# Optimization experiments

Measured on AMD Instinct MI355X. Metric: run time of the kernel, lower is better.

The kernel has to match this reference:

```python
import jax, jax.numpy as jnp
import numpy as np

LPB = 0.03   # lower_probability_bound
LEB = 0.2    # lower_entropy_bound
UEB = 0.5    # upper_entropy_bound
BETA = 1.0
N, K, S, D = 8192, 1000, 8, 1024


def setup_inputs() -> dict:
    key = jax.random.key(0)
    k1, k2, k3 = jax.random.split(key, 3)
    x = jax.random.normal(k1, (N, D), dtype=jnp.float32)
    # per-sample logit temperature so entropies spread across the gating band
    base = jax.random.normal(k2, (N, K), dtype=jnp.float32)
    scales = jax.random.uniform(k3, (N, 1), dtype=jnp.float32, minval=1.0, maxval=15.0)
    text_logits = base * scales
    memory = jnp.zeros((K, S, D), dtype=jnp.float32)
    # init_entropy(prop_max=1): -log(1/K) = log(K)
    memory_entropy = jnp.full((K, S), jnp.log(jnp.float32(K)), dtype=jnp.float32)
    memory_state = jnp.zeros((K, S), dtype=bool)
    return {"x": x, "text_logits": text_logits, "memory": memory,
            "memory_entropy": memory_entropy, "memory_state": memory_state}


def _update_memory(memory, memory_entropy, memory_state, x, text_logits):
    """Sequential entropy-gated scatter update (order-dependent, as in torch loop)."""
    def step(carry, inp):
        mem, ent, st = carry
        xi, li = inp                      # xi: [D], li: [K]
        p = jax.nn.softmax(li)
        lab = jnp.argmax(li)
        H = -jnp.sum(jnp.log(p + 1e-6) * p)  # shannon entropy
        row = ent[lab]                    # [S] entropies of this class's slots
        cond = (p[lab] > LPB) & (H > LEB) & (H < UEB) & jnp.any(H < row)
        idx = jnp.argmax(row)             # evict highest-entropy slot
        mem = mem.at[lab, idx].set(jnp.where(cond, xi, mem[lab, idx]))
        ent = ent.at[lab, idx].set(jnp.where(cond, H, ent[lab, idx]))
        st = st.at[lab, idx].set(jnp.where(cond, True, st[lab, idx]))
        return (mem, ent, st), cond

    (mem, ent, st), selected = jax.lax.scan(
        step, (memory, memory_entropy, memory_state), (x, text_logits))
    return mem, ent, st, selected


def reference(x, text_logits, memory, memory_entropy, memory_state):
    mem, ent, st, selected = _update_memory(memory, memory_entropy, memory_state, x, text_logits)
    # get_logits: A_ = (memory @ x.T).permute(2,0,1) -> [N, K, S]
    A_ = jnp.einsum('ksd,nd->nks', mem, x)
    logits = -jnp.sum(jnp.exp(-BETA * (1.0 - A_)), axis=-1)  # [N, K]
    return logits
```

## Files before the change

### kernel.cpp

```cpp
#include <hip/hip_runtime.h>
#include <hip/hip_bf16.h>
#include <math.h>

#define NN 8192
#define KK 1000
#define SS 8
#define DD 1024
#define RR (KK * SS)
#define RRP 8192

typedef __bf16 bf16x8 __attribute__((ext_vector_type(8)));
typedef float f32x4 __attribute__((ext_vector_type(4)));
typedef unsigned short ushort_t;
typedef ushort_t ushort8 __attribute__((ext_vector_type(8)));

static __device__ __forceinline__ ushort_t f2bf(float f) {
  unsigned u = __float_as_uint(f);
  unsigned r = (u + 0x7FFFu + ((u >> 16) & 1u)) >> 16;
  return (ushort_t)r;
}

#define GLD16(gsrc, ldst)                                                     \
  __builtin_amdgcn_global_load_lds(                                           \
      (const __attribute__((address_space(1))) unsigned int*)(gsrc),          \
      (__attribute__((address_space(3))) unsigned int*)(ldst), 16, 0, 0)

#define SBAR() asm volatile("s_barrier" ::: "memory")
#define WAITVM(n) asm volatile("s_waitcnt vmcnt(" #n ")" ::: "memory")

__global__ __launch_bounds__(256) void stats_kernel(
    const float* __restrict__ tl, int2* __restrict__ cand) {
  __shared__ float sv[KK];
  __shared__ float redv[256];
  __shared__ int   redi[256];
  const int n = blockIdx.x;
  const int t = threadIdx.x;
  const float* row = tl + (size_t)n * KK;
  for (int j = t; j < KK; j += 256) sv[j] = row[j];
  __syncthreads();

  float bv = -INFINITY; int bi = KK;
  for (int j = t; j < KK; j += 256) { float v = sv[j]; if (v > bv) { bv = v; bi = j; } }
  redv[t] = bv; redi[t] = bi;
  __syncthreads();
  for (int off = 128; off > 0; off >>= 1) {
    if (t < off) {
      float ov = redv[t + off]; int oi = redi[t + off];
      if (ov > redv[t] || (ov == redv[t] && oi < redi[t])) { redv[t] = ov; redi[t] = oi; }
    }
    __syncthreads();
  }
  const float m = redv[0];
  const int lab = redi[0];
  __syncthreads();

  float z = 0.f;
  for (int j = t; j < KK; j += 256) z += expf(sv[j] - m);
  redv[t] = z;
  __syncthreads();
  for (int off = 128; off > 0; off >>= 1) {
    if (t < off) redv[t] += redv[t + off];
    __syncthreads();
  }
  const float Z = redv[0];
  __syncthreads();

  float h = 0.f;
  for (int j = t; j < KK; j += 256) {
    float p = expf(sv[j] - m) / Z;
    h -= p * logf(p + 1e-6f);
  }
  redv[t] = h;
  __syncthreads();
  for (int off = 128; off > 0; off >>= 1) {
    if (t < off) redv[t] += redv[t + off];
    __syncthreads();
  }
  if (t == 0) {
    const float H = redv[0];
    const float plab = 1.0f / Z;
    const bool c = (plab > 0.03f) && (H > 0.2f) && (H < 0.5f);
    cand[n] = make_int2(c ? lab : -1, __float_as_int(H));
  }
}

__global__ __launch_bounds__(256) void select_kernel(
    const int2* __restrict__ cand, const float* __restrict__ ment,
    int* __restrict__ sel) {
  const int w = threadIdx.x >> 6;
  const int l = threadIdx.x & 63;
  const int k = blockIdx.x * 4 + w;
  if (k >= KK) return;

  float ent[SS]; int idx[SS];
  #pragma unroll
  for (int s = 0; s < SS; ++s) { ent[s] = ment[k * SS + s]; idx[s] = -1; }

  for (int base = 0; base < NN; base += 64) {
    const int2 c = cand[base + l];
    unsigned long long msk = __ballot(c.x == k);
    while (msk) {
      const int src = __ffsll((long long)msk) - 1;
      msk &= msk - 1;
      const float H = __shfl(__int_as_float(c.y), src);
      float mx = ent[0]; int mi = 0;
      #pragma unroll
      for (int s = 1; s < SS; ++s) if (ent[s] > mx) { mx = ent[s]; mi = s; }
      if (H < mx) { ent[mi] = H; idx[mi] = base + src; }
    }
  }
  if (l == 0) {
    #pragma unroll
    for (int s = 0; s < SS; ++s) sel[k * SS + s] = idx[s];
  }
}

__global__ __launch_bounds__(128) void convgather_kernel(
    const float* __restrict__ x, const float* __restrict__ mem,
    const int* __restrict__ sel, ushort_t* __restrict__ xb,
    ushort_t* __restrict__ Bb) {
  const int r = blockIdx.x;
  const int t = threadIdx.x;
  const float* src;
  ushort_t* dst;
  if (r < NN) {
    src = x + (size_t)r * DD;
    dst = xb + (size_t)r * DD;
  } else {
    const int rr = r - NN;
    dst = Bb + (size_t)rr * DD;
    if (rr >= RR) {
      *(ushort8*)(dst + t * 8) = (ushort8)0;
      return;
    }
    const int sl = sel[rr];
    src = (sl >= 0) ? (x + (size_t)sl * DD) : (mem + (size_t)rr * DD);
  }
  const float4 a = *(const float4*)(src + t * 8);
  const float4 b = *(const float4*)(src + t * 8 + 4);
  ushort8 o;
  o[0] = f2bf(a.x); o[1] = f2bf(a.y); o[2] = f2bf(a.z); o[3] = f2bf(a.w);
  o[4] = f2bf(b.x); o[5] = f2bf(b.y); o[6] = f2bf(b.z); o[7] = f2bf(b.w);
  *(ushort8*)(dst + t * 8) = o;
}

#define BKT 32
#define NT (DD / BKT)

__global__ __launch_bounds__(512, 2) void logits_kernel(
    const ushort_t* __restrict__ xb, const ushort_t* __restrict__ Bb,
    float* __restrict__ out) {
  __shared__ ushort_t lds[2 * 16384];
  const int t = threadIdx.x;
  const int w = t >> 6;
  const int l = t & 63;
  const int wm = w >> 2;
  const int wn = w & 3;
  const int n0 = blockIdx.x * 256;
  const int r0 = blockIdx.y * 256;

  const int srow = w * 16 + (l >> 2);
  const int schunkh = (((l & 3) ^ ((l >> 3) & 3)) << 3);
  const ushort_t* gA0 = xb + (size_t)(n0 + srow) * DD + schunkh;
  const ushort_t* gA1 = xb + (size_t)(n0 + srow + 128) * DD + schunkh;
  const ushort_t* gB0 = Bb + (size_t)(r0 + srow) * DD + schunkh;
  const ushort_t* gB1 = Bb + (size_t)(r0 + srow + 128) * DD + schunkh;

#define STAGE_A(T, p) do {                                                    \
    GLD16(gA0 + (size_t)(T) * BKT, lds + (p) * 16384 + w * 512);              \
    GLD16(gA1 + (size_t)(T) * BKT, lds + (p) * 16384 + 4096 + w * 512);       \
  } while (0)
#define STAGE_B(T, p) do {                                                    \
    GLD16(gB0 + (size_t)(T) * BKT, lds + (p) * 16384 + 8192 + w * 512);       \
    GLD16(gB1 + (size_t)(T) * BKT, lds + (p) * 16384 + 12288 + w * 512);      \
  } while (0)

  const int lr = l & 15;
  const int ch = l >> 4;
  const int swz = ((ch ^ ((lr >> 1) & 3)) << 3);
  const int Aoff = (wm * 128 + lr) * 32 + swz;
  const int Boff = 8192 + (wn * 64 + lr) * 32 + swz;

  f32x4 acc[8][4];
  #pragma unroll
  for (int mi = 0; mi < 8; ++mi)
    #pragma unroll
    for (int ni = 0; ni < 4; ++ni) acc[mi][ni] = (f32x4){0.f, 0.f, 0.f, 0.f};

  STAGE_A(0, 0); STAGE_B(0, 0);
  WAITVM(0);
  SBAR();

  #pragma unroll 2
  for (int T = 0; T < NT; ++T) {
    const int p = T & 1;
    const ushort_t* buf = lds + p * 16384;
    bf16x8 af0[4], af1[4], bfr[4];

    if (T + 1 < NT) { STAGE_A(T + 1, (T + 1) & 1); STAGE_B(T + 1, (T + 1) & 1); }

    #pragma unroll
    for (int mi = 0; mi < 4; ++mi)
      af0[mi] = *(const bf16x8*)(buf + Aoff + mi * 512);
    #pragma unroll
    for (int ni = 0; ni < 4; ++ni)
      bfr[ni] = *(const bf16x8*)(buf + Boff + ni * 512);
    #pragma unroll
    for (int mi = 0; mi < 4; ++mi)
      af1[mi] = *(const bf16x8*)(buf + Aoff + 2048 + mi * 512);

    __builtin_amdgcn_s_setprio(1);
    #pragma unroll
    for (int mi = 0; mi < 4; ++mi)
      #pragma unroll
      for (int ni = 0; ni < 4; ++ni)
        acc[mi][ni] = __builtin_amdgcn_mfma_f32_16x16x32_bf16(
            af0[mi], bfr[ni], acc[mi][ni], 0, 0, 0);
    #pragma unroll
    for (int mi = 0; mi < 4; ++mi)
      #pragma unroll
      for (int ni = 0; ni < 4; ++ni)
        acc[mi + 4][ni] = __builtin_amdgcn_mfma_f32_16x16x32_bf16(
            af1[mi], bfr[ni], acc[mi + 4][ni], 0, 0, 0);
    __builtin_amdgcn_s_setprio(0);

    WAITVM(0);
    SBAR();
  }

  const int rbase = n0 + wm * 128 + ((l >> 4) * 4);
  #pragma unroll
  for (int mi = 0; mi < 8; ++mi) {
    #pragma unroll
    for (int ni = 0; ni < 4; ++ni) {
      const int colbase = r0 + wn * 64 + ni * 16 + (l & 15);
      const int cls = colbase >> 3;
      #pragma unroll
      for (int rg = 0; rg < 4; ++rg) {
        float e = __expf(acc[mi][ni][rg] - 1.0f);
        e += __shfl_xor(e, 1);
        e += __shfl_xor(e, 2);
        e += __shfl_xor(e, 4);
        if ((l & 7) == 0 && cls < KK) {
          out[(size_t)(rbase + mi * 16 + rg) * KK + cls] = -fminf(e, 3.0e38f);
        }
      }
    }
  }
}

extern "C" void kernel_launch(void* const* d_in, const int* in_sizes, int n_in,
                              void* d_out, int out_size, void* d_ws, size_t ws_size,
                              hipStream_t stream) {
  const float* x    = (const float*)d_in[0];
  const float* tl   = (const float*)d_in[1];
  const float* mem  = (const float*)d_in[2];
  const float* ment = (const float*)d_in[3];
  float* out = (float*)d_out;

  char* ws = (char*)d_ws;
  int2*     cand = (int2*)ws;
  int*      sel  = (int*)(ws + NN * 8);
  ushort_t* Bb   = (ushort_t*)(ws + (1 << 20));
  ushort_t* xb   = (ushort_t*)(ws + (1 << 20) + (size_t)RRP * DD * 2);

  hipLaunchKernelGGL(stats_kernel, dim3(NN), dim3(256), 0, stream, tl, cand);
  hipLaunchKernelGGL(select_kernel, dim3(250), dim3(256), 0, stream, cand, ment, sel);
  hipLaunchKernelGGL(convgather_kernel, dim3(NN + RRP), dim3(128), 0, stream,
                     x, mem, sel, xb, Bb);
  hipLaunchKernelGGL(logits_kernel, dim3(32, 32), dim3(512), 0, stream, xb, Bb, out);
}
```

Before: 241.5 us.

## Double BK to 64 and interleave chunked async staging with MFMA clusters

Raises the GEMM K-tile from 32 to 64 with a new 8-chunk XOR swizzle. Next-tile global-to-LDS loads are split into per-64-row chunks and issued between four MFMA clusters, gated by partial vmcnt waits and sched_barriers. The goal is to hide global load latency behind MFMA work instead of waiting for the whole tile each iteration. In exchange, LDS use doubles to 128 KB per block, which likely allows only one block per CU despite launch_bounds(512,2), and each iteration now has more barriers.

```diff
diff --git a/kernel.cpp b/kernel.cpp
--- a/kernel.cpp
+++ b/kernel.cpp
@@ -144,13 +144,14 @@
   *(ushort8*)(dst + t * 8) = o;
 }
 
-#define BKT 32
-#define NT (DD / BKT)
+#define BKS 64
+#define NTS (DD / BKS)
+#define LDSH 32768
 
 __global__ __launch_bounds__(512, 2) void logits_kernel(
     const ushort_t* __restrict__ xb, const ushort_t* __restrict__ Bb,
     float* __restrict__ out) {
-  __shared__ ushort_t lds[2 * 16384];
+  __shared__ ushort_t lds[2 * LDSH];
   const int t = threadIdx.x;
   const int w = t >> 6;
   const int l = t & 63;
@@ -159,27 +160,24 @@
   const int n0 = blockIdx.x * 256;
   const int r0 = blockIdx.y * 256;
 
-  const int srow = w * 16 + (l >> 2);
-  const int schunkh = (((l & 3) ^ ((l >> 3) & 3)) << 3);
-  const ushort_t* gA0 = xb + (size_t)(n0 + srow) * DD + schunkh;
-  const ushort_t* gA1 = xb + (size_t)(n0 + srow + 128) * DD + schunkh;
-  const ushort_t* gB0 = Bb + (size_t)(r0 + srow) * DD + schunkh;
-  const ushort_t* gB1 = Bb + (size_t)(r0 + srow + 128) * DD + schunkh;
-
-#define STAGE_A(T, p) do {                                                    \
-    GLD16(gA0 + (size_t)(T) * BKT, lds + (p) * 16384 + w * 512);              \
-    GLD16(gA1 + (size_t)(T) * BKT, lds + (p) * 16384 + 4096 + w * 512);       \
-  } while (0)
-#define STAGE_B(T, p) do {                                                    \
-    GLD16(gB0 + (size_t)(T) * BKT, lds + (p) * 16384 + 8192 + w * 512);       \
-    GLD16(gB1 + (size_t)(T) * BKT, lds + (p) * 16384 + 12288 + w * 512);      \
-  } while (0)
+  const int srow = w * 8 + (l >> 3);
+  const int gcolh = (((l & 7) ^ ((l >> 3) & 7)) << 3);
+  const ushort_t* gA = xb + (size_t)(n0 + srow) * DD + gcolh;
+  const ushort_t* gB = Bb + (size_t)(r0 + srow) * DD + gcolh;
+
+#define STAGE_AC(T, c)                                                        \
+  GLD16(gA + (size_t)(c) * 64 * DD + (size_t)(T) * BKS,                       \
+        lds + ((T) & 1) * LDSH + (c) * 4096 + w * 512)
+#define STAGE_BC(T, c)                                                        \
+  GLD16(gB + (size_t)(c) * 64 * DD + (size_t)(T) * BKS,                       \
+        lds + ((T) & 1) * LDSH + 16384 + (c) * 4096 + w * 512)
 
   const int lr = l & 15;
   const int ch = l >> 4;
-  const int swz = ((ch ^ ((lr >> 1) & 3)) << 3);
-  const int Aoff = (wm * 128 + lr) * 32 + swz;
-  const int Boff = 8192 + (wn * 64 + lr) * 32 + swz;
+  const int kc0 = ((ch ^ (lr & 7)) << 3);
+  const int kc1 = (((4 + ch) ^ (lr & 7)) << 3);
+  const int arow = (wm * 128 + lr) * 64;
+  const int brow = 16384 + (wn * 64 + lr) * 64;
 
   f32x4 acc[8][4];
   #pragma unroll
@@ -187,44 +185,82 @@
     #pragma unroll
     for (int ni = 0; ni < 4; ++ni) acc[mi][ni] = (f32x4){0.f, 0.f, 0.f, 0.f};
 
-  STAGE_A(0, 0); STAGE_B(0, 0);
-  WAITVM(0);
+  STAGE_AC(0, 0); STAGE_AC(0, 2);
+  STAGE_BC(0, 0); STAGE_BC(0, 2);
+  STAGE_BC(0, 1); STAGE_BC(0, 3);
+  STAGE_AC(0, 1); STAGE_AC(0, 3);
+  WAITVM(2);
   SBAR();
 
+#define MFMA_CLUSTER(q)                                                       \
+  do {                                                                        \
+    __builtin_amdgcn_sched_barrier(0);                                        \
+    __builtin_amdgcn_s_setprio(1);                                            \
+    _Pragma("unroll")                                                         \
+    for (int i = 0; i < 2; ++i)                                               \
+      _Pragma("unroll")                                                       \
+      for (int ni = 0; ni < 4; ++ni)                                          \
+        acc[2 * (q) + i][ni] = __builtin_amdgcn_mfma_f32_16x16x32_bf16(       \
+            af[i][0], bf[ni][0], acc[2 * (q) + i][ni], 0, 0, 0);              \
+    _Pragma("unroll")                                                         \
+    for (int i = 0; i < 2; ++i)                                               \
+      _Pragma("unroll")                                                       \
+      for (int ni = 0; ni < 4; ++ni)                                          \
+        acc[2 * (q) + i][ni] = __builtin_amdgcn_mfma_f32_16x16x32_bf16(       \
+            af[i][1], bf[ni][1], acc[2 * (q) + i][ni], 0, 0, 0);              \
+    __builtin_amdgcn_s_setprio(0);                                            \
+    __builtin_amdgcn_sched_barrier(0);                                        \
+  } while (0)
+
   #pragma unroll 2
-  for (int T = 0; T < NT; ++T) {
-    const int p = T & 1;
-    const ushort_t* buf = lds + p * 16384;
-    bf16x8 af0[4], af1[4], bfr[4];
-
-    if (T + 1 < NT) { STAGE_A(T + 1, (T + 1) & 1); STAGE_B(T + 1, (T + 1) & 1); }
+  for (int T = 0; T < NTS; ++T) {
+    const ushort_t* buf = lds + (T & 1) * LDSH;
+    const int Tn = T + 1;
+    const bool st = (Tn < NTS);
+    bf16x8 bf[4][2];
+    bf16x8 af[2][2];
 
     #pragma unroll
-    for (int mi = 0; mi < 4; ++mi)
-      af0[mi] = *(const bf16x8*)(buf + Aoff + mi * 512);
-    #pragma unroll
-    for (int ni = 0; ni < 4; ++ni)
-      bfr[ni] = *(const bf16x8*)(buf + Boff + ni * 512);
-    #pragma unroll
-    for (int mi = 0; mi < 4; ++mi)
-      af1[mi] = *(const bf16x8*)(buf + Aoff + 2048 + mi * 512);
-
-    __builtin_amdgcn_s_setprio(1);
-    #pragma unroll
-    for (int mi = 0; mi < 4; ++mi)
-      #pragma unroll
-      for (int ni = 0; ni < 4; ++ni)
-        acc[mi][ni] = __builtin_amdgcn_mfma_f32_16x16x32_bf16(
-            af0[mi], bfr[ni], acc[mi][ni], 0, 0, 0);
-    #pragma unroll
-    for (int mi = 0; mi < 4; ++mi)
-      #pragma unroll
-      for (int ni = 0; ni < 4; ++ni)
-        acc[mi + 4][ni] = __builtin_amdgcn_mfma_f32_16x16x32_bf16(
-            af1[mi], bfr[ni], acc[mi + 4][ni], 0, 0, 0);
-    __builtin_amdgcn_s_setprio(0);
-
-    WAITVM(0);
+    for (int ni = 0; ni < 4; ++ni) {
+      bf[ni][0] = *(const bf16x8*)(buf + brow + ni * 1024 + kc0);
+      bf[ni][1] = *(const bf16x8*)(buf + brow + ni * 1024 + kc1);
+    }
+    af[0][0] = *(const bf16x8*)(buf + arow + kc0);
+    af[0][1] = *(const bf16x8*)(buf + arow + kc1);
+    af[1][0] = *(const bf16x8*)(buf + arow + 1024 + kc0);
+    af[1][1] = *(const bf16x8*)(buf + arow + 1024 + kc1);
+    if (st) { STAGE_AC(Tn, 0); STAGE_AC(Tn, 2); }
+    SBAR();
+    MFMA_CLUSTER(0);
+    SBAR();
+
+    af[0][0] = *(const bf16x8*)(buf + arow + 2048 + kc0);
+    af[0][1] = *(const bf16x8*)(buf + arow + 2048 + kc1);
+    af[1][0] = *(const bf16x8*)(buf + arow + 3072 + kc0);
+    af[1][1] = *(const bf16x8*)(buf + arow + 3072 + kc1);
+    if (st) { STAGE_BC(Tn, 0); STAGE_BC(Tn, 2); }
+    SBAR();
+    MFMA_CLUSTER(1);
+    SBAR();
+
+    if (T < NTS - 1) { WAITVM(4); } else { WAITVM(0); }
+    af[0][0] = *(const bf16x8*)(buf + arow + 4096 + kc0);
+    af[0][1] = *(const bf16x8*)(buf + arow + 4096 + kc1);
+    af[1][0] = *(const bf16x8*)(buf + arow + 5120 + kc0);
+    af[1][1] = *(const bf16x8*)(buf + arow + 5120 + kc1);
+    if (st) { STAGE_BC(Tn, 1); STAGE_BC(Tn, 3); }
+    SBAR();
+    MFMA_CLUSTER(2);
+    SBAR();
+
+    af[0][0] = *(const bf16x8*)(buf + arow + 6144 + kc0);
+    af[0][1] = *(const bf16x8*)(buf + arow + 6144 + kc1);
+    af[1][0] = *(const bf16x8*)(buf + arow + 7168 + kc0);
+    af[1][1] = *(const bf16x8*)(buf + arow + 7168 + kc1);
+    if (st) { STAGE_AC(Tn, 1); STAGE_AC(Tn, 3); }
+    SBAR();
+    MFMA_CLUSTER(3);
+    WAITVM(2);
     SBAR();
   }
 
```

Result: faster. 235.4 us (-2.5%).
